# Performance work log

Measured on AMD Instinct MI355X. Metric: run time of the kernel, lower is better.

## Reference

```python
import jax, jax.numpy as jnp
import numpy as np


def setup_inputs() -> dict:
    key = jax.random.key(0)
    ks = jax.random.split(key, 8)
    N, E, F, H = 50000, 400000, 128, 512
    x = jax.random.normal(ks[0], (N, F), dtype=jnp.float32)
    edge_index = jax.random.randint(ks[1], (2, E), 0, N, dtype=jnp.int32)
    W1 = jax.random.normal(ks[2], (H, 2 * F), dtype=jnp.float32) * 0.05
    b1 = jax.random.normal(ks[3], (H,), dtype=jnp.float32) * 0.05
    W2 = jax.random.normal(ks[4], (H, 2 * H), dtype=jnp.float32) * 0.05
    b2 = jax.random.normal(ks[5], (H,), dtype=jnp.float32) * 0.05
    Wo = jax.random.normal(ks[6], (1, H), dtype=jnp.float32) * 0.05
    bo = jax.random.normal(ks[7], (1,), dtype=jnp.float32) * 0.05
    return {"x": x, "edge_index": edge_index, "W1": W1, "b1": b1,
            "W2": W2, "b2": b2, "Wo": Wo, "bo": bo}


def reference(x, edge_index, W1, b1, W2, b2, Wo, bo):
    # GraphSAGE mean aggregation: agg[dst] = mean over incoming edges of h[src]
    N = x.shape[0]
    src = edge_index[0]
    dst = edge_index[1]
    deg = jax.ops.segment_sum(jnp.ones_like(dst, dtype=x.dtype), dst,
                              num_segments=N)
    inv_deg = 1.0 / jnp.maximum(deg, 1.0)  # clamp_min(1.0)

    def agg_mean(h):
        s = jax.ops.segment_sum(h[src], dst, num_segments=N)  # [N, D]
        return s * inv_deg[:, None]

    # Layer 1: concat(self, neigh) -> Linear -> ReLU (dropout = identity, eval)
    n1 = agg_mean(x)
    h1 = jax.nn.relu(jnp.concatenate([x, n1], axis=1) @ W1.T + b1)
    # Layer 2
    n2 = agg_mean(h1)
    h2 = jax.nn.relu(jnp.concatenate([h1, n2], axis=1) @ W2.T + b2)
    # Output head
    logits = h2 @ Wo.T + bo  # [N, 1]
    return jax.nn.sigmoid(logits)
```

## Files before the change

kernel.cpp:

```cpp
#include <hip/hip_runtime.h>
#include <math.h>


typedef __attribute__((ext_vector_type(8))) short bf16x8;
typedef __attribute__((ext_vector_type(4))) float f32x4;

static inline int ceil_div(int a, int b) { return (a + b - 1) / b; }

__device__ inline float bf2f_lo(unsigned u) { return __builtin_bit_cast(float, u << 16); }
__device__ inline float bf2f_hi(unsigned u) { return __builtin_bit_cast(float, u & 0xffff0000u); }
__device__ inline unsigned f2bf(float f) {
    unsigned u = __builtin_bit_cast(unsigned, f);
    u += 0x7fffu + ((u >> 16) & 1u);
    return u >> 16;
}

#define GLOAD_LDS16(gp, lp)                                                   \
    __builtin_amdgcn_global_load_lds(                                         \
        (__attribute__((address_space(1))) void*)(gp),                        \
        (__attribute__((address_space(3))) void*)(lp), 16, 0, 0)


__global__ void cvt3_hist_kernel(const float* __restrict__ a, unsigned short* __restrict__ ao, int na4,
                                 const float* __restrict__ b, unsigned short* __restrict__ bo, int nb4,
                                 const float* __restrict__ c, unsigned short* __restrict__ co, int nc4,
                                 const int* __restrict__ dst, int* __restrict__ deg, int E,
                                 int cvt_blocks) {
    if ((int)blockIdx.x < cvt_blocks) {
        int i = blockIdx.x * 256 + threadIdx.x;
        const float* in; unsigned short* out; int k;
        if (i < na4)                  { in = a; out = ao; k = i; }
        else if (i < na4 + nb4)       { in = b; out = bo; k = i - na4; }
        else if (i < na4 + nb4 + nc4) { in = c; out = co; k = i - na4 - nb4; }
        else return;
        float4 v = ((const float4*)in)[k];
        ushort4 o;
        o.x = (unsigned short)f2bf(v.x);
        o.y = (unsigned short)f2bf(v.y);
        o.z = (unsigned short)f2bf(v.z);
        o.w = (unsigned short)f2bf(v.w);
        ((ushort4*)out)[k] = o;
    } else {
        int e = (blockIdx.x - cvt_blocks) * 256 + threadIdx.x;
        if (e < E) atomicAdd(&deg[dst[e]], 1);
    }
}


__global__ __launch_bounds__(256) void chunk_reduce(const int* __restrict__ deg,
                                                    int* __restrict__ partial, int N) {
    int base = blockIdx.x * 1024;
    int s = 0;
    for (int i = threadIdx.x; i < 1024; i += 256) {
        int idx = base + i;
        if (idx < N) s += deg[idx];
    }
    #pragma unroll
    for (int off = 32; off; off >>= 1) s += __shfl_down(s, off);
    __shared__ int ws[4];
    if ((threadIdx.x & 63) == 0) ws[threadIdx.x >> 6] = s;
    __syncthreads();
    if (threadIdx.x == 0) partial[blockIdx.x] = ws[0] + ws[1] + ws[2] + ws[3];
}

__global__ void partial_scan(int* __restrict__ partial, int* __restrict__ rowstartN, int P) {
    int lane = threadIdx.x;
    int v = (lane < P) ? partial[lane] : 0;
    int incl = v;
    #pragma unroll
    for (int off = 1; off < 64; off <<= 1) {
        int t = __shfl_up(incl, off);
        if (lane >= off) incl += t;
    }
    if (lane < P) partial[lane] = incl - v;
    if (lane == 63) *rowstartN = incl;
}

__global__ __launch_bounds__(256) void chunk_scan(const int* __restrict__ deg,
                                                  const int* __restrict__ partial,
                                                  int* __restrict__ rowstart,
                                                  int* __restrict__ cursor, int N) {
    int base = blockIdx.x * 1024 + threadIdx.x * 4;
    int v[4];
    #pragma unroll
    for (int j = 0; j < 4; ++j) {
        int i = base + j;
        v[j] = (i < N) ? deg[i] : 0;
    }
    int mysum = v[0] + v[1] + v[2] + v[3];
    int incl = mysum;
    int lane = threadIdx.x & 63, wave = threadIdx.x >> 6;
    #pragma unroll
    for (int off = 1; off < 64; off <<= 1) {
        int t = __shfl_up(incl, off);
        if (lane >= off) incl += t;
    }
    __shared__ int ws[4];
    if (lane == 63) ws[wave] = incl;
    __syncthreads();
    int run = partial[blockIdx.x] + incl - mysum;
    for (int w = 0; w < wave; ++w) run += ws[w];
    #pragma unroll
    for (int j = 0; j < 4; ++j) {
        int i = base + j;
        if (i < N) { rowstart[i] = run; cursor[i] = run; }
        run += v[j];
    }
}

__global__ void bucket_kernel(const int* __restrict__ src, const int* __restrict__ dst,
                              int* __restrict__ cursor, int* __restrict__ ebuf, int E) {
    int e = blockIdx.x * 256 + threadIdx.x;
    if (e < E) {
        int pos = atomicAdd(&cursor[dst[e]], 1);
        ebuf[pos] = src[e];
    }
}


__global__ void gather_mean_128(const int* __restrict__ rowstart, const int* __restrict__ ebuf,
                                const unsigned* __restrict__ featb, unsigned* __restrict__ outb, int N) {
    int w = (blockIdx.x * blockDim.x + threadIdx.x) >> 6;
    int lane = threadIdx.x & 63;
    if (w >= N) return;
    int e0 = rowstart[w], e1 = rowstart[w + 1];
    float ax = 0.0f, ay = 0.0f;
    int i = e0;
    for (; i + 8 <= e1; i += 8) {
        unsigned v0 = featb[(size_t)ebuf[i]     * 64 + lane];
        unsigned v1 = featb[(size_t)ebuf[i + 1] * 64 + lane];
        unsigned v2 = featb[(size_t)ebuf[i + 2] * 64 + lane];
        unsigned v3 = featb[(size_t)ebuf[i + 3] * 64 + lane];
        unsigned v4 = featb[(size_t)ebuf[i + 4] * 64 + lane];
        unsigned v5 = featb[(size_t)ebuf[i + 5] * 64 + lane];
        unsigned v6 = featb[(size_t)ebuf[i + 6] * 64 + lane];
        unsigned v7 = featb[(size_t)ebuf[i + 7] * 64 + lane];
        ax += bf2f_lo(v0) + bf2f_lo(v1) + bf2f_lo(v2) + bf2f_lo(v3)
            + bf2f_lo(v4) + bf2f_lo(v5) + bf2f_lo(v6) + bf2f_lo(v7);
        ay += bf2f_hi(v0) + bf2f_hi(v1) + bf2f_hi(v2) + bf2f_hi(v3)
            + bf2f_hi(v4) + bf2f_hi(v5) + bf2f_hi(v6) + bf2f_hi(v7);
    }
    for (; i < e1; ++i) {
        unsigned v = featb[(size_t)ebuf[i] * 64 + lane];
        ax += bf2f_lo(v); ay += bf2f_hi(v);
    }
    float inv = 1.0f / fmaxf((float)(e1 - e0), 1.0f);
    outb[(size_t)w * 64 + lane] = f2bf(ax * inv) | (f2bf(ay * inv) << 16);
}

__global__ void gather_mean_512(const int* __restrict__ rowstart, const int* __restrict__ ebuf,
                                const unsigned short* __restrict__ featb,
                                unsigned short* __restrict__ outb, int N) {
    int w = (blockIdx.x * blockDim.x + threadIdx.x) >> 6;
    int lane = threadIdx.x & 63;
    if (w >= N) return;
    int e0 = rowstart[w], e1 = rowstart[w + 1];
    float a[8] = {0, 0, 0, 0, 0, 0, 0, 0};
    const uint4* base = (const uint4*)featb;
    int i = e0;
    for (; i + 8 <= e1; i += 8) {
        uint4 v0 = base[(size_t)ebuf[i]     * 64 + lane];
        uint4 v1 = base[(size_t)ebuf[i + 1] * 64 + lane];
        uint4 v2 = base[(size_t)ebuf[i + 2] * 64 + lane];
        uint4 v3 = base[(size_t)ebuf[i + 3] * 64 + lane];
        uint4 v4 = base[(size_t)ebuf[i + 4] * 64 + lane];
        uint4 v5 = base[(size_t)ebuf[i + 5] * 64 + lane];
        uint4 v6 = base[(size_t)ebuf[i + 6] * 64 + lane];
        uint4 v7 = base[(size_t)ebuf[i + 7] * 64 + lane];
        a[0] += bf2f_lo(v0.x) + bf2f_lo(v1.x) + bf2f_lo(v2.x) + bf2f_lo(v3.x)
              + bf2f_lo(v4.x) + bf2f_lo(v5.x) + bf2f_lo(v6.x) + bf2f_lo(v7.x);
        a[1] += bf2f_hi(v0.x) + bf2f_hi(v1.x) + bf2f_hi(v2.x) + bf2f_hi(v3.x)
              + bf2f_hi(v4.x) + bf2f_hi(v5.x) + bf2f_hi(v6.x) + bf2f_hi(v7.x);
        a[2] += bf2f_lo(v0.y) + bf2f_lo(v1.y) + bf2f_lo(v2.y) + bf2f_lo(v3.y)
              + bf2f_lo(v4.y) + bf2f_lo(v5.y) + bf2f_lo(v6.y) + bf2f_lo(v7.y);
        a[3] += bf2f_hi(v0.y) + bf2f_hi(v1.y) + bf2f_hi(v2.y) + bf2f_hi(v3.y)
              + bf2f_hi(v4.y) + bf2f_hi(v5.y) + bf2f_hi(v6.y) + bf2f_hi(v7.y);
        a[4] += bf2f_lo(v0.z) + bf2f_lo(v1.z) + bf2f_lo(v2.z) + bf2f_lo(v3.z)
              + bf2f_lo(v4.z) + bf2f_lo(v5.z) + bf2f_lo(v6.z) + bf2f_lo(v7.z);
        a[5] += bf2f_hi(v0.z) + bf2f_hi(v1.z) + bf2f_hi(v2.z) + bf2f_hi(v3.z)
              + bf2f_hi(v4.z) + bf2f_hi(v5.z) + bf2f_hi(v6.z) + bf2f_hi(v7.z);
        a[6] += bf2f_lo(v0.w) + bf2f_lo(v1.w) + bf2f_lo(v2.w) + bf2f_lo(v3.w)
              + bf2f_lo(v4.w) + bf2f_lo(v5.w) + bf2f_lo(v6.w) + bf2f_lo(v7.w);
        a[7] += bf2f_hi(v0.w) + bf2f_hi(v1.w) + bf2f_hi(v2.w) + bf2f_hi(v3.w)
              + bf2f_hi(v4.w) + bf2f_hi(v5.w) + bf2f_hi(v6.w) + bf2f_hi(v7.w);
    }
    for (; i < e1; ++i) {
        uint4 v = base[(size_t)ebuf[i] * 64 + lane];
        a[0] += bf2f_lo(v.x); a[1] += bf2f_hi(v.x);
        a[2] += bf2f_lo(v.y); a[3] += bf2f_hi(v.y);
        a[4] += bf2f_lo(v.z); a[5] += bf2f_hi(v.z);
        a[6] += bf2f_lo(v.w); a[7] += bf2f_hi(v.w);
    }
    float inv = 1.0f / fmaxf((float)(e1 - e0), 1.0f);
    uint4 o;
    o.x = f2bf(a[0] * inv) | (f2bf(a[1] * inv) << 16);
    o.y = f2bf(a[2] * inv) | (f2bf(a[3] * inv) << 16);
    o.z = f2bf(a[4] * inv) | (f2bf(a[5] * inv) << 16);
    o.w = f2bf(a[6] * inv) | (f2bf(a[7] * inv) << 16);
    ((uint4*)outb)[(size_t)w * 64 + lane] = o;
}

__global__ __launch_bounds__(256) void gemm_mfma(
    const unsigned short* __restrict__ A0,
    const unsigned short* __restrict__ A1,
    const unsigned short* __restrict__ W,
    const float* __restrict__ b,
    unsigned short* __restrict__ outb,
    const float* __restrict__ Wo,
    float* __restrict__ logit,
    int N, int K0, int K1, int C, int mode)
{
    const int nrow = (N + 127) >> 7;
    const int id   = blockIdx.x;
    const int rowb = ((id >> 5) << 3) + (id & 7);
    const int colb = (id >> 3) & 3;
    if (rowb >= nrow) return;

    const int K = K0 + K1;
    const int S = K0;
    __shared__ short As[2][4096];
    __shared__ short Bs[2][4096];

    const int tid  = threadIdx.x;
    const int lane = tid & 63;
    const int wave = tid >> 6;
    const int wm = wave & 1, wn = wave >> 1;
    const int cl = lane & 15, quad = lane >> 4;
    const int row0 = rowb * 128;
    const int col0 = colb * 128;

    const int r = lane >> 2;
    const int j = lane & 3;
    const int trow0 = wave * 32 + r;
    const int trow1 = trow0 + 16;
    const int ar0 = (row0 + trow0 < N) ? row0 + trow0 : N - 1;
    const int ar1 = (row0 + trow1 < N) ? row0 + trow1 : N - 1;
    const size_t aoff0 = (size_t)ar0 * S + j * 8;
    const size_t aoff1 = (size_t)ar1 * S + j * 8;
    const size_t boff0 = (size_t)(col0 + trow0) * K + j * 8;
    const size_t boff1 = (size_t)(col0 + trow1) * K + j * 8;
    const int lds0 = (wave * 32) * 32;
    const int lds1 = (wave * 32 + 16) * 32;

    f32x4 acc[4][4];
    #pragma unroll
    for (int mt = 0; mt < 4; ++mt)
        #pragma unroll
        for (int nt = 0; nt < 4; ++nt)
            acc[mt][nt] = (f32x4){0.f, 0.f, 0.f, 0.f};

    GLOAD_LDS16(A0 + aoff0, &As[0][lds0]);
    GLOAD_LDS16(A0 + aoff1, &As[0][lds1]);
    GLOAD_LDS16(W  + boff0, &Bs[0][lds0]);
    GLOAD_LDS16(W  + boff1, &Bs[0][lds1]);

    const int iters = K >> 5;
    for (int i = 0; i < iters; ++i) {
        const int cur = i & 1;
        __syncthreads();
        if (i + 1 < iters) {
            const int kn = (i + 1) << 5;
            const unsigned short* Ab = (kn < K0) ? (A0 + kn) : (A1 + (kn - K0));
            const unsigned short* Wb = W + kn;
            const int nb = cur ^ 1;
            GLOAD_LDS16(Ab + aoff0, &As[nb][lds0]);
            GLOAD_LDS16(Ab + aoff1, &As[nb][lds1]);
            GLOAD_LDS16(Wb + boff0, &Bs[nb][lds0]);
            GLOAD_LDS16(Wb + boff1, &Bs[nb][lds1]);
        }

        bf16x8 af[4], bfr[4];
        #pragma unroll
        for (int mt = 0; mt < 4; ++mt)
            af[mt] = *(const bf16x8*)&As[cur][(wm * 64 + mt * 16 + cl) * 32 + quad * 8];
        #pragma unroll
        for (int nt = 0; nt < 4; ++nt)
            bfr[nt] = *(const bf16x8*)&Bs[cur][(wn * 64 + nt * 16 + cl) * 32 + quad * 8];

        #pragma unroll
        for (int mt = 0; mt < 4; ++mt)
            #pragma unroll
            for (int nt = 0; nt < 4; ++nt)
                acc[mt][nt] = __builtin_amdgcn_mfma_f32_16x16x32_bf16(
                    af[mt], bfr[nt], acc[mt][nt], 0, 0, 0);
    }

    if (mode == 0) {
        #pragma unroll
        for (int nt = 0; nt < 4; ++nt) {
            const int colx = col0 + wn * 64 + nt * 16 + cl;
            const float bb = b[colx];
            #pragma unroll
            for (int mt = 0; mt < 4; ++mt) {
                #pragma unroll
                for (int rr = 0; rr < 4; ++rr) {
                    int row = row0 + wm * 64 + mt * 16 + quad * 4 + rr;
                    if (row < N)
                        outb[(size_t)row * C + colx] =
                            (unsigned short)f2bf(fmaxf(acc[mt][nt][rr] + bb, 0.0f));
                }
            }
        }
    } else {
        float bv[4], wv2[4];
        #pragma unroll
        for (int nt = 0; nt < 4; ++nt) {
            const int colx = col0 + wn * 64 + nt * 16 + cl;
            bv[nt] = b[colx];
            wv2[nt] = Wo[colx];
        }
        #pragma unroll
        for (int mt = 0; mt < 4; ++mt) {
            #pragma unroll
            for (int rr = 0; rr < 4; ++rr) {
                float s = 0.0f;
                #pragma unroll
                for (int nt = 0; nt < 4; ++nt)
                    s += fmaxf(acc[mt][nt][rr] + bv[nt], 0.0f) * wv2[nt];
                s += __shfl_xor(s, 1);
                s += __shfl_xor(s, 2);
                s += __shfl_xor(s, 4);
                s += __shfl_xor(s, 8);
                int row = row0 + wm * 64 + mt * 16 + quad * 4 + rr;
                if (cl == 0 && row < N) atomicAdd(&logit[row], s);
            }
        }
    }
}

__global__ void head_kernel(const float* __restrict__ logit, const float* __restrict__ bo,
                            float* __restrict__ out, int N) {
    int i = blockIdx.x * 256 + threadIdx.x;
    if (i < N) out[i] = 1.0f / (1.0f + expf(-(logit[i] + bo[0])));
}

extern "C" void kernel_launch(void* const* d_in, const int* in_sizes, int n_in,
                              void* d_out, int out_size, void* d_ws, size_t ws_size,
                              hipStream_t stream) {
    const float* x  = (const float*)d_in[0];
    const int*   ei = (const int*)d_in[1];
    const float* W1 = (const float*)d_in[2];
    const float* b1 = (const float*)d_in[3];
    const float* W2 = (const float*)d_in[4];
    const float* b2 = (const float*)d_in[5];
    const float* Wo = (const float*)d_in[6];
    const float* bo = (const float*)d_in[7];
    float* out = (float*)d_out;

    const int N = in_sizes[0] / 128;
    const int E = in_sizes[1] / 2;
    const int* src = ei;
    const int* dst = ei + E;

    char* ws = (char*)d_ws;
    size_t off = 0;
    auto alloc = [&](size_t bytes) {
        void* p = ws + off;
        off += (bytes + 255) & ~(size_t)255;
        return p;
    };
    int* deg      = (int*)alloc((size_t)N * 4);
    int* rowstart = (int*)alloc((size_t)(N + 1) * 4);
    int* cursor   = (int*)alloc((size_t)N * 4);
    int* partial  = (int*)alloc((size_t)64 * 4);
    int* ebuf     = (int*)alloc((size_t)E * 4);
    float* logit  = (float*)alloc((size_t)N * 4);
    unsigned short* xb  = (unsigned short*)alloc((size_t)N * 128 * 2);
    unsigned short* W1b = (unsigned short*)alloc((size_t)512 * 256 * 2);
    unsigned short* W2b = (unsigned short*)alloc((size_t)512 * 1024 * 2);
    unsigned short* n1b = (unsigned short*)alloc((size_t)N * 128 * 2);
    unsigned short* h1b = (unsigned short*)alloc((size_t)N * 512 * 2);
    unsigned short* n2b = (unsigned short*)alloc((size_t)N * 512 * 2);
    (void)ws_size; (void)n_in; (void)out_size;

    hipMemsetAsync(deg,   0, (size_t)N * 4, stream);
    hipMemsetAsync(logit, 0, (size_t)N * 4, stream);

    const int na4 = N * 128 / 4, nb4 = 512 * 256 / 4, nc4 = 512 * 1024 / 4;
    const int cvt_blocks  = ceil_div(na4 + nb4 + nc4, 256);
    const int hist_blocks = ceil_div(E, 256);
    cvt3_hist_kernel<<<cvt_blocks + hist_blocks, 256, 0, stream>>>(
        x, xb, na4, W1, W1b, nb4, W2, W2b, nc4, dst, deg, E, cvt_blocks);

    const int P = ceil_div(N, 1024);
    chunk_reduce<<<P, 256, 0, stream>>>(deg, partial, N);
    partial_scan<<<1, 64, 0, stream>>>(partial, rowstart + N, P);
    chunk_scan<<<P, 256, 0, stream>>>(deg, partial, rowstart, cursor, N);
    bucket_kernel<<<ceil_div(E, 256), 256, 0, stream>>>(src, dst, cursor, ebuf, E);

    const int nrow = ceil_div(N, 128);
    const int gblocks = ceil_div(nrow, 8) * 8 * 4;

    gather_mean_128<<<ceil_div(N * 64, 256), 256, 0, stream>>>(rowstart, ebuf,
                                                               (const unsigned*)xb, (unsigned*)n1b, N);
    gemm_mfma<<<gblocks, 256, 0, stream>>>(xb, n1b, W1b, b1, h1b, nullptr, nullptr,
                                           N, 128, 128, 512, 0);

    gather_mean_512<<<ceil_div(N * 64, 256), 256, 0, stream>>>(rowstart, ebuf, h1b, n2b, N);
    gemm_mfma<<<gblocks, 256, 0, stream>>>(h1b, n2b, W2b, b2, nullptr, Wo, logit,
                                           N, 512, 512, 512, 1);

    head_kernel<<<ceil_div(N, 256), 256, 0, stream>>>(logit, bo, out, N);
}
```

Before: 350.5 us.

## Replace layer-2 GEMM with 256x256-tile 8-phase pipelined MFMA kernel

Adds a dedicated layer-2 GEMM kernel with 512 threads, 256x256 output tiles and a 128KB double-buffered LDS pipeline. Global-to-LDS loads are interleaved with MFMA phases under explicit barriers, waitcnts and priority hints. The fused bias/ReLU/Wo-dot epilogue is kept. The goal is to hide memory latency and raise MFMA utilisation in the largest GEMM. The trade-offs are heavy LDS use that limits occupancy and a hardcoded K=1024 and N=512 layout.

```diff
diff --git a/kernel.cpp b/kernel.cpp
--- a/kernel.cpp
+++ b/kernel.cpp
@@ -328,6 +328,189 @@
     }
 }
 
+
+#define KT2  16
+#define NIT2 8
+
+#define STG_A(hh, kt, buf) do {                                                        \
+    const unsigned short* _pA = ((kt) < 8) ? A0 : A1;                                  \
+    const size_t _ko = (size_t)(((kt) & 7) << 6);                                      \
+    GLOAD_LDS16(_pA + _ko + offA[hh][0],                                               \
+                lds + (buf) * 65536 + (hh) * 16384 + (w * 2 + 0) * 1024);              \
+    GLOAD_LDS16(_pA + _ko + offA[hh][1],                                               \
+                lds + (buf) * 65536 + (hh) * 16384 + (w * 2 + 1) * 1024);              \
+} while (0)
+
+#define STG_B(hh, kt, buf) do {                                                        \
+    const size_t _ko = (size_t)((kt) << 6);                                            \
+    GLOAD_LDS16(W + _ko + offB[hh][0],                                                 \
+                lds + (buf) * 65536 + 32768 + (hh) * 16384 + (w * 2 + 0) * 1024);      \
+    GLOAD_LDS16(W + _ko + offB[hh][1],                                                 \
+                lds + (buf) * 65536 + 32768 + (hh) * 16384 + (w * 2 + 1) * 1024);      \
+} while (0)
+
+#define RD_A8(qm, buf) do {                                                            \
+    _Pragma("unroll")                                                                  \
+    for (int _m = 0; _m < 4; ++_m) {                                                   \
+        af[_m][0] = *(const bf16x8*)(lds + (buf) * 65536 +                             \
+                    ((aBase + ((qm) * 4 + _m) * 2048) ^ swz));                         \
+        af[_m][1] = *(const bf16x8*)(lds + (buf) * 65536 +                             \
+                    ((aBase + ((qm) * 4 + _m) * 2048 + 64) ^ swz));                    \
+    }                                                                                  \
+} while (0)
+
+#define RD_B4(qn, buf) do {                                                            \
+    _Pragma("unroll")                                                                  \
+    for (int _n = 0; _n < 2; ++_n) {                                                   \
+        bq[(qn) * 2 + _n][0] = *(const bf16x8*)(lds + (buf) * 65536 +                  \
+                    ((bBase + ((qn) * 2 + _n) * 2048) ^ swz));                         \
+        bq[(qn) * 2 + _n][1] = *(const bf16x8*)(lds + (buf) * 65536 +                  \
+                    ((bBase + ((qn) * 2 + _n) * 2048 + 64) ^ swz));                    \
+    }                                                                                  \
+} while (0)
+
+#define MFMA16(qm, qn) do {                                                            \
+    _Pragma("unroll")                                                                  \
+    for (int _kk = 0; _kk < 2; ++_kk)                                                  \
+        _Pragma("unroll")                                                              \
+        for (int _m = 0; _m < 4; ++_m)                                                 \
+            _Pragma("unroll")                                                          \
+            for (int _n = 0; _n < 2; ++_n)                                             \
+                acc[(qm) * 4 + _m][(qn) * 2 + _n] =                                    \
+                    __builtin_amdgcn_mfma_f32_16x16x32_bf16(                           \
+                        af[_m][_kk], bq[(qn) * 2 + _n][_kk],                           \
+                        acc[(qm) * 4 + _m][(qn) * 2 + _n], 0, 0, 0);                   \
+} while (0)
+
+#define PH_SYNC_MFMA(qm, qn) do {                                                      \
+    __builtin_amdgcn_sched_barrier(0);                                                 \
+    __builtin_amdgcn_s_barrier();                                                      \
+    __builtin_amdgcn_sched_barrier(0);                                                 \
+    asm volatile("s_waitcnt lgkmcnt(0)" ::: "memory");                                 \
+    __builtin_amdgcn_s_setprio(1);                                                     \
+    MFMA16(qm, qn);                                                                    \
+    __builtin_amdgcn_s_setprio(0);                                                     \
+    __builtin_amdgcn_sched_barrier(0);                                                 \
+    __builtin_amdgcn_s_barrier();                                                      \
+    __builtin_amdgcn_sched_barrier(0);                                                 \
+} while (0)
+
+__global__ __launch_bounds__(512, 2) void gemm2_8ph(
+    const unsigned short* __restrict__ A0,
+    const unsigned short* __restrict__ A1,
+    const unsigned short* __restrict__ W,
+    const float* __restrict__ b,
+    const float* __restrict__ Wo,
+    float* __restrict__ logit,
+    int N)
+{
+    __shared__ char lds[131072];
+
+    const int nrt = (N + 255) >> 8;
+    const int nb  = nrt * 2;
+    const int orig = blockIdx.x;
+    int virt = orig;
+    if ((nb & 7) == 0) virt = (orig & 7) * (nb >> 3) + (orig >> 3);
+    const int row0 = (virt >> 1) << 8;
+    const int col0 = (virt & 1) << 8;
+
+    const int tid = threadIdx.x;
+    const int w = tid >> 6, l = tid & 63;
+    const int wr = w >> 2, wc = w & 3;
+    const int cl = l & 15, quad = l >> 4;
+
+    const int c_log = ((l & 7) * 8) ^ ((l >> 5) << 4);
+    size_t offA[2][2], offB[2][2];
+    #pragma unroll
+    for (int hh = 0; hh < 2; ++hh)
+        #pragma unroll
+        for (int i = 0; i < 2; ++i) {
+            int ra = row0 + hh * 128 + (w * 2 + i) * 8 + (l >> 3);
+            if (ra > N - 1) ra = N - 1;
+            offA[hh][i] = (size_t)ra * 512 + c_log;
+            const int rb = col0 + hh * 128 + (w * 2 + i) * 8 + (l >> 3);
+            offB[hh][i] = (size_t)rb * 1024 + c_log;
+        }
+
+    const int swz   = (cl & 4) << 3;
+    const int aBase = wr * 16384 + cl * 128 + quad * 16;
+    const int bBase = 32768 + (wc * 64 + cl) * 128 + quad * 16;
+
+    f32x4 acc[8][4];
+    #pragma unroll
+    for (int mt = 0; mt < 8; ++mt)
+        #pragma unroll
+        for (int nt = 0; nt < 4; ++nt)
+            acc[mt][nt] = (f32x4){0.f, 0.f, 0.f, 0.f};
+
+    bf16x8 af[4][2];
+    bf16x8 bq[4][2];
+
+    STG_A(0, 0, 0); STG_A(1, 0, 0);
+    STG_B(0, 0, 0); STG_B(1, 0, 0);
+    STG_B(0, 1, 1); STG_B(1, 1, 1);
+    asm volatile("s_waitcnt vmcnt(4)" ::: "memory");
+    __builtin_amdgcn_s_barrier();
+    __builtin_amdgcn_sched_barrier(0);
+
+    for (int j = 0; j < NIT2; ++j) {
+        const int t1 = 2 * j + 1;
+        const int t2 = (2 * j + 2 < KT2) ? 2 * j + 2 : KT2 - 2;
+        const int t3 = (2 * j + 3 < KT2) ? 2 * j + 3 : KT2 - 1;
+        RD_A8(0, 0); RD_B4(0, 0);
+        STG_A(0, t1, 1);
+        asm volatile("s_waitcnt lgkmcnt(8)" ::: "memory");
+        PH_SYNC_MFMA(0, 0);
+        RD_B4(1, 0);
+        STG_A(1, t1, 1);
+        PH_SYNC_MFMA(0, 1);
+        RD_A8(1, 0);
+        STG_B(0, t2, 0);
+        PH_SYNC_MFMA(1, 1);
+        STG_B(1, t2, 0);
+        asm volatile("s_waitcnt vmcnt(4)" ::: "memory");
+        PH_SYNC_MFMA(1, 0);
+        RD_A8(0, 1); RD_B4(0, 1);
+        STG_A(0, t2, 0);
+        asm volatile("s_waitcnt lgkmcnt(8)" ::: "memory");
+        PH_SYNC_MFMA(0, 0);
+        RD_B4(1, 1);
+        STG_A(1, t2, 0);
+        PH_SYNC_MFMA(0, 1);
+        RD_A8(1, 1);
+        STG_B(0, t3, 1);
+        PH_SYNC_MFMA(1, 1);
+        STG_B(1, t3, 1);
+        asm volatile("s_waitcnt vmcnt(4)" ::: "memory");
+        PH_SYNC_MFMA(1, 0);
+    }
+    asm volatile("s_waitcnt vmcnt(0)" ::: "memory");
+
+    float bv[4], wv[4];
+    #pragma unroll
+    for (int nt = 0; nt < 4; ++nt) {
+        const int colx = col0 + wc * 64 + nt * 16 + cl;
+        bv[nt] = b[colx];
+        wv[nt] = Wo[colx];
+    }
+    #pragma unroll
+    for (int mt = 0; mt < 8; ++mt) {
+        #pragma unroll
+        for (int rr = 0; rr < 4; ++rr) {
+            float s = 0.0f;
+            #pragma unroll
+            for (int nt = 0; nt < 4; ++nt)
+                s += fmaxf(acc[mt][nt][rr] + bv[nt], 0.0f) * wv[nt];
+            s += __shfl_xor(s, 1);
+            s += __shfl_xor(s, 2);
+            s += __shfl_xor(s, 4);
+            s += __shfl_xor(s, 8);
+            const int row = row0 + wr * 128 + mt * 16 + quad * 4 + rr;
+            if (cl == 0 && row < N) atomicAdd(&logit[row], s);
+        }
+    }
+}
+
 __global__ void head_kernel(const float* __restrict__ logit, const float* __restrict__ bo,
                             float* __restrict__ out, int N) {
     int i = blockIdx.x * 256 + threadIdx.x;
@@ -390,15 +573,14 @@
 
     const int nrow = ceil_div(N, 128);
     const int gblocks = ceil_div(nrow, 8) * 8 * 4;
-
     gather_mean_128<<<ceil_div(N * 64, 256), 256, 0, stream>>>(rowstart, ebuf,
                                                                (const unsigned*)xb, (unsigned*)n1b, N);
     gemm_mfma<<<gblocks, 256, 0, stream>>>(xb, n1b, W1b, b1, h1b, nullptr, nullptr,
                                            N, 128, 128, 512, 0);
 
     gather_mean_512<<<ceil_div(N * 64, 256), 256, 0, stream>>>(rowstart, ebuf, h1b, n2b, N);
-    gemm_mfma<<<gblocks, 256, 0, stream>>>(h1b, n2b, W2b, b2, nullptr, Wo, logit,
-                                           N, 512, 512, 512, 1);
+    const int nrt2 = ceil_div(N, 256);
+    gemm2_8ph<<<nrt2 * 2, 512, 0, stream>>>(h1b, n2b, W2b, b2, Wo, logit, N);
 
     head_kernel<<<ceil_div(N, 256), 256, 0, stream>>>(logit, bo, out, N);
 }
```

Measured after the change: 345.8 us. About the same (-1.3%).

## Add triple-buffered 128x256-tile MFMA GEMM for layer-2 with fused head

Applied to the files above, without the earlier changes.

Replaces the generic layer-2 GEMM with a dedicated kernel that computes 128x256 output tiles using 8 waves, a three-stage LDS ring filled via global_load_lds, and an XCD-aware block remapping. Each K-step waits on a partial vmcnt so loads for step t+2 overlap the MFMAs of step t, and s_setprio raises the priority of MFMA issue. The bias, ReLU and output-projection epilogue with atomic logit accumulation is kept. The larger tile and 72KB LDS footprint reduce A-operand reloads but limit occupancy, and the hand-tuned waitcnt gating depends on the exact load counts.

```diff
diff --git a/kernel.cpp b/kernel.cpp
--- a/kernel.cpp
+++ b/kernel.cpp
@@ -328,6 +328,127 @@
     }
 }
 
+
+#define KT3 32
+
+#define STG3(kt) do {                                                          \
+    const unsigned short* _p = ((kt) < 16) ? (A0 + ((kt) << 5))                \
+                                           : (A1 + (((kt) - 16) << 5));        \
+    const int _bf = (kt) % 3;                                                  \
+    GLOAD_LDS16(_p + offA, lds + _bf * 8192 + w * 1024);                       \
+    GLOAD_LDS16(W + ((kt) << 5) + offB0,                                       \
+                lds + 24576 + _bf * 16384 + w * 2048);                         \
+    GLOAD_LDS16(W + ((kt) << 5) + offB1,                                       \
+                lds + 24576 + _bf * 16384 + w * 2048 + 1024);                  \
+} while (0)
+
+#define RD3(bf) do {                                                           \
+    _Pragma("unroll")                                                          \
+    for (int _m = 0; _m < 4; ++_m)                                             \
+        af[_m] = *(const bf16x8*)(lds + (bf) * 8192 + aoff + _m * 1024);       \
+    _Pragma("unroll")                                                          \
+    for (int _n = 0; _n < 4; ++_n)                                             \
+        bq[_n] = *(const bf16x8*)(lds + 24576 + (bf) * 16384 + boff + _n * 1024); \
+} while (0)
+
+#define MM16() do {                                                            \
+    _Pragma("unroll")                                                          \
+    for (int _m = 0; _m < 4; ++_m)                                             \
+        _Pragma("unroll")                                                      \
+        for (int _n = 0; _n < 4; ++_n)                                         \
+            acc[_m][_n] = __builtin_amdgcn_mfma_f32_16x16x32_bf16(             \
+                af[_m], bq[_n], acc[_m][_n], 0, 0, 0);                         \
+} while (0)
+
+#define PHASE3(t, stage, gatestr) do {                                         \
+    __builtin_amdgcn_sched_barrier(0);                                         \
+    asm volatile("s_waitcnt " gatestr ::: "memory");                           \
+    __builtin_amdgcn_s_barrier();                                              \
+    __builtin_amdgcn_sched_barrier(0);                                         \
+    RD3((t) % 3);                                                              \
+    if (stage) STG3((t) + 2);                                                  \
+    __builtin_amdgcn_s_setprio(1);                                             \
+    MM16();                                                                    \
+    __builtin_amdgcn_s_setprio(0);                                             \
+} while (0)
+
+__global__ __launch_bounds__(512, 4) void gemm2_3buf(
+    const unsigned short* __restrict__ A0,
+    const unsigned short* __restrict__ A1,
+    const unsigned short* __restrict__ W,
+    const float* __restrict__ b,
+    const float* __restrict__ Wo,
+    float* __restrict__ logit,
+    int N)
+{
+    __shared__ char lds[73728];
+
+    const int nwg  = ((N + 127) >> 7) * 2;
+    const int orig = blockIdx.x;
+    const int xcd = orig & 7, lnum = orig >> 3;
+    const int q = nwg >> 3, r = nwg & 7;
+    const int virt = (xcd < r ? xcd * (q + 1) : r * (q + 1) + (xcd - r) * q) + lnum;
+    const int row0 = (virt >> 1) << 7;
+    const int col0 = (virt & 1) << 8;
+
+    const int tid = threadIdx.x;
+    const int w = tid >> 6, l = tid & 63;
+    const int wr = w >> 2, wc = w & 3;
+    const int cl = l & 15, quad = l >> 4;
+
+    const int c_log = (((l & 3) ^ ((l >> 3) & 3))) * 8;
+    int ra = row0 + w * 16 + (l >> 2);
+    if (ra > N - 1) ra = N - 1;
+    const size_t offA  = (size_t)ra * 512 + c_log;
+    const size_t offB0 = (size_t)(col0 + w * 32 + (l >> 2)) * 1024 + c_log;
+    const size_t offB1 = (size_t)(col0 + w * 32 + 16 + (l >> 2)) * 1024 + c_log;
+
+    const int swz  = ((cl >> 1) & 3) << 4;
+    const int aoff = (((wr * 64 + cl) * 64) + quad * 16) ^ swz;
+    const int boff = (((wc * 64 + cl) * 64) + quad * 16) ^ swz;
+
+    f32x4 acc[4][4];
+    #pragma unroll
+    for (int mt = 0; mt < 4; ++mt)
+        #pragma unroll
+        for (int nt = 0; nt < 4; ++nt)
+            acc[mt][nt] = (f32x4){0.f, 0.f, 0.f, 0.f};
+
+    bf16x8 af[4], bq[4];
+
+    STG3(0); STG3(1);
+
+    #pragma unroll
+    for (int t = 0; t < 30; ++t)
+        PHASE3(t, 1, "vmcnt(3)");
+    PHASE3(30, 0, "vmcnt(3)");
+    PHASE3(31, 0, "vmcnt(0)");
+
+    float bv[4], wv[4];
+    #pragma unroll
+    for (int nt = 0; nt < 4; ++nt) {
+        const int colx = col0 + wc * 64 + nt * 16 + cl;
+        bv[nt] = b[colx];
+        wv[nt] = Wo[colx];
+    }
+    #pragma unroll
+    for (int mt = 0; mt < 4; ++mt) {
+        #pragma unroll
+        for (int rr = 0; rr < 4; ++rr) {
+            float s = 0.0f;
+            #pragma unroll
+            for (int nt = 0; nt < 4; ++nt)
+                s += fmaxf(acc[mt][nt][rr] + bv[nt], 0.0f) * wv[nt];
+            s += __shfl_xor(s, 1);
+            s += __shfl_xor(s, 2);
+            s += __shfl_xor(s, 4);
+            s += __shfl_xor(s, 8);
+            const int row = row0 + wr * 64 + mt * 16 + quad * 4 + rr;
+            if (cl == 0 && row < N) atomicAdd(&logit[row], s);
+        }
+    }
+}
+
 __global__ void head_kernel(const float* __restrict__ logit, const float* __restrict__ bo,
                             float* __restrict__ out, int N) {
     int i = blockIdx.x * 256 + threadIdx.x;
@@ -390,15 +511,14 @@
 
     const int nrow = ceil_div(N, 128);
     const int gblocks = ceil_div(nrow, 8) * 8 * 4;
-
     gather_mean_128<<<ceil_div(N * 64, 256), 256, 0, stream>>>(rowstart, ebuf,
                                                                (const unsigned*)xb, (unsigned*)n1b, N);
     gemm_mfma<<<gblocks, 256, 0, stream>>>(xb, n1b, W1b, b1, h1b, nullptr, nullptr,
                                            N, 128, 128, 512, 0);
 
     gather_mean_512<<<ceil_div(N * 64, 256), 256, 0, stream>>>(rowstart, ebuf, h1b, n2b, N);
-    gemm_mfma<<<gblocks, 256, 0, stream>>>(h1b, n2b, W2b, b2, nullptr, Wo, logit,
-                                           N, 512, 512, 512, 1);
+    const int g2 = ceil_div(N, 128) * 2;
+    gemm2_3buf<<<g2, 512, 0, stream>>>(h1b, n2b, W2b, b2, Wo, logit, N);
 
     head_kernel<<<ceil_div(N, 256), 256, 0, stream>>>(logit, bo, out, N);
 }
```

New measurement: 335.5 us. 4.3% less time.
